# Optimization experiments

Hardware: AMD Instinct MI355X
Metric: run time of the kernel (lower is better)

The kernel has to match this reference:

```python
import jax, jax.numpy as jnp
import numpy as np

E, R, D, B = 1_000_000, 1_000, 64, 32_768
MARGIN = 1.0


def setup_inputs() -> dict:
    key = jax.random.key(0)
    ks = jax.random.split(key, 8)
    return {
        "ent_embeddings": jax.random.normal(ks[0], (E, D), dtype=jnp.float32) * (1.0 / np.sqrt(D)),
        "rel_matrices": jax.random.normal(ks[1], (R, D * D), dtype=jnp.float32) * (1.0 / D),
        "ph": jax.random.randint(ks[2], (B,), 0, E, dtype=jnp.int32),
        "pt": jax.random.randint(ks[3], (B,), 0, E, dtype=jnp.int32),
        "pr": jax.random.randint(ks[4], (B,), 0, R, dtype=jnp.int32),
        "nh": jax.random.randint(ks[5], (B,), 0, E, dtype=jnp.int32),
        "nt": jax.random.randint(ks[6], (B,), 0, E, dtype=jnp.int32),
        "nr": jax.random.randint(ks[7], (B,), 0, R, dtype=jnp.int32),
    }


def _score(ent, rel, h_idx, t_idx, r_idx):
    # gather: h,t -> [B,D]; r -> [B,D,D]
    h = ent[h_idx]
    t = ent[t_idx]
    r = rel[r_idx].reshape(-1, D, D)
    rt = jnp.einsum('bij,bj->bi', r, t)      # matmul(pr, pt): [B,D]
    # mean over D (keep_dims=False) then sum keepdims -> [B,1]
    return jnp.mean(h * rt, axis=1, keepdims=True)


def reference(ent_embeddings, rel_matrices, ph, pt, pr, nh, nt, nr):
    sp = _score(ent_embeddings, rel_matrices, ph, pt, pr)  # [B,1]
    sn = _score(ent_embeddings, rel_matrices, nh, nt, nr)  # [B,1]
    return jnp.sum(jnp.maximum(0.0, sn - sp + MARGIN))
```

## Files before the change

### kernel.cpp

```cpp
#include <hip/hip_runtime.h>


#define DIM 64
#define BATCH 32768
#define NREL 1000
#define NTASK (2 * BATCH)
#define BINCAP 128
#define RS 68
#define TS 36


__global__ __launch_bounds__(256) void scatter_kernel(
    const int* __restrict__ pr, const int* __restrict__ nr,
    int* __restrict__ cursors, int* __restrict__ bins,
    float* __restrict__ out)
{
    int t = blockIdx.x * 256 + threadIdx.x;
    int b = t & (BATCH - 1);
    int r = (t >> 15) ? nr[b] : pr[b];
    int c = atomicAdd(&cursors[r], 1);
    if (c < BINCAP) bins[r * BINCAP + c] = t;
    if (blockIdx.x == 0 && threadIdx.x == 0) *out = 0.f;
}

__global__ __launch_bounds__(256) void score_kernel(
    const float* __restrict__ ent, const float* __restrict__ rel,
    const int* __restrict__ ph, const int* __restrict__ pt,
    const int* __restrict__ nh, const int* __restrict__ nt,
    const int* __restrict__ cursors, const int* __restrict__ bins,
    float* __restrict__ scores)
{
    const int r = blockIdx.x;
    const int w = threadIdx.x >> 6;
    const int lane = threadIdx.x & 63;

    __shared__ float RT[DIM * RS];
    __shared__ float TT[4 * DIM * TS];

    const float4* rg = (const float4*)(rel + (size_t)r * (DIM * DIM));
    #pragma unroll
    for (int it = 0; it < 4; ++it) {
        int f = threadIdx.x + 256 * it;
        int i = f >> 4, jc = f & 15;
        float4 v = rg[f];
        RT[(4 * jc + 0) * RS + i] = v.x;
        RT[(4 * jc + 1) * RS + i] = v.y;
        RT[(4 * jc + 2) * RS + i] = v.z;
        RT[(4 * jc + 3) * RS + i] = v.w;
    }

    const int start = r * BINCAP;
    const int cnt = min(cursors[r], BINCAP);
    const int tb = start + w * 32;
    const int nv = min(32, cnt - w * 32);

    float* tt = &TT[w * (DIM * TS)];
    if (nv > 0) {
        int m = lane & 31;
        int ch = lane >> 5;
        int t = bins[tb + min(m, nv - 1)];
        int b = t & (BATCH - 1);
        int ti = (t >> 15) ? nt[b] : pt[b];
        const float4* tr = (const float4*)(ent + (size_t)ti * DIM);
        #pragma unroll
        for (int c = 0; c < 8; ++c) {
            float4 v = tr[ch * 8 + c];
            int j = ch * 32 + c * 4;
            tt[(j + 0) * TS + m] = v.x;
            tt[(j + 1) * TS + m] = v.y;
            tt[(j + 2) * TS + m] = v.z;
            tt[(j + 3) * TS + m] = v.w;
        }
    }
    __syncthreads();
    if (nv <= 0) return;

    const int mg = lane >> 3;
    const int ig = lane & 7;

    float acc[4][8];
    #pragma unroll
    for (int a = 0; a < 4; ++a)
        #pragma unroll
        for (int b = 0; b < 8; ++b) acc[a][b] = 0.f;

    const float* ttA = tt + mg * 4;
    const float* rtB = RT + ig * 8;
    #pragma unroll 2
    for (int j = 0; j < 64; ++j) {
        float4 Av = *(const float4*)(ttA + j * TS);
        float4 B0 = *(const float4*)(rtB + j * RS);
        float4 B1 = *(const float4*)(rtB + j * RS + 4);
        float A_[4] = {Av.x, Av.y, Av.z, Av.w};
        float B_[8] = {B0.x, B0.y, B0.z, B0.w, B1.x, B1.y, B1.z, B1.w};
        #pragma unroll
        for (int a = 0; a < 4; ++a)
            #pragma unroll
            for (int b = 0; b < 8; ++b)
                acc[a][b] = fmaf(A_[a], B_[b], acc[a][b]);
    }

    float sc[4]; int tk[4];
    #pragma unroll
    for (int a = 0; a < 4; ++a) {
        int m = mg * 4 + a;
        int t = bins[tb + min(m, nv - 1)];
        tk[a] = t;
        int b = t & (BATCH - 1);
        int hi = (t >> 15) ? nh[b] : ph[b];
        const float4* hr = (const float4*)(ent + (size_t)hi * DIM);
        float4 h0 = hr[ig * 2];
        float4 h1 = hr[ig * 2 + 1];
        float p = h0.x * acc[a][0] + h0.y * acc[a][1] +
                  h0.z * acc[a][2] + h0.w * acc[a][3] +
                  h1.x * acc[a][4] + h1.y * acc[a][5] +
                  h1.z * acc[a][6] + h1.w * acc[a][7];
        p += __shfl_xor(p, 1, 64);
        p += __shfl_xor(p, 2, 64);
        p += __shfl_xor(p, 4, 64);
        sc[a] = p;
    }
    if (ig == 0) {
        #pragma unroll
        for (int a = 0; a < 4; ++a)
            if (mg * 4 + a < nv) scores[tk[a]] = sc[a] * (1.0f / DIM);
    }
}

__global__ __launch_bounds__(256) void hinge_kernel(
    const float* __restrict__ scores, float* __restrict__ out)
{
    int b = blockIdx.x * 256 + threadIdx.x;
    float sp = scores[b];
    float sn = scores[BATCH + b];
    float v = fmaxf(0.f, sn - sp + 1.0f);
    #pragma unroll
    for (int off = 32; off > 0; off >>= 1)
        v += __shfl_xor(v, off, 64);
    __shared__ float red[4];
    int warp = threadIdx.x >> 6;
    int lane = threadIdx.x & 63;
    if (lane == 0) red[warp] = v;
    __syncthreads();
    if (threadIdx.x == 0)
        atomicAdd(out, red[0] + red[1] + red[2] + red[3]);
}

extern "C" void kernel_launch(void* const* d_in, const int* in_sizes, int n_in,
                              void* d_out, int out_size, void* d_ws, size_t ws_size,
                              hipStream_t stream) {
    const float* ent = (const float*)d_in[0];
    const float* rel = (const float*)d_in[1];
    const int* ph = (const int*)d_in[2];
    const int* pt = (const int*)d_in[3];
    const int* pr = (const int*)d_in[4];
    const int* nh = (const int*)d_in[5];
    const int* nt = (const int*)d_in[6];
    const int* nr = (const int*)d_in[7];
    float* out = (float*)d_out;

    char* ws = (char*)d_ws;
    int* cursors  = (int*)(ws + 0);
    int* bins     = (int*)(ws + 4096);
    float* scores = (float*)(ws + 516096);

    hipMemsetAsync(cursors, 0, 4096, stream);
    scatter_kernel<<<NTASK / 256, 256, 0, stream>>>(pr, nr, cursors, bins, out);
    score_kernel<<<NREL, 256, 0, stream>>>(ent, rel, ph, pt, nh, nt,
                                           cursors, bins, scores);
    hinge_kernel<<<BATCH / 256, 256, 0, stream>>>(scores, out);
}
```

Before: 341.9 us.

## Fuse hinge reduction into score kernel and pack gather indices into bins

The scatter kernel now stores the task id, tail index and head index together in an int4 bin entry. This removes the dependent index loads from the score kernel, which also issues its head-row loads before the matmul loop. The separate hinge kernel and scores buffer are gone: each triple's score is paired with its positive or negative partner through an atomicExch on a sentinel-initialised slot, and the hinge value is reduced per block into out. This saves a kernel launch and the scores round trip, at the cost of larger bin entries and extra global atomics.

```diff
diff --git a/kernel.cpp b/kernel.cpp
--- a/kernel.cpp
+++ b/kernel.cpp
@@ -8,27 +8,32 @@
 #define BINCAP 128
 #define RS 68
 #define TS 36
+#define SENT 0x7F800001u
 
 
 __global__ __launch_bounds__(256) void scatter_kernel(
-    const int* __restrict__ pr, const int* __restrict__ nr,
-    int* __restrict__ cursors, int* __restrict__ bins,
-    float* __restrict__ out)
+    const int* __restrict__ ph, const int* __restrict__ pt,
+    const int* __restrict__ pr, const int* __restrict__ nh,
+    const int* __restrict__ nt, const int* __restrict__ nr,
+    int* __restrict__ cursors, int4* __restrict__ bins,
+    unsigned int* __restrict__ pairs, float* __restrict__ out)
 {
     int t = blockIdx.x * 256 + threadIdx.x;
     int b = t & (BATCH - 1);
-    int r = (t >> 15) ? nr[b] : pr[b];
+    int side = t >> 15;
+    int r  = side ? nr[b] : pr[b];
+    int ti = side ? nt[b] : pt[b];
+    int hi = side ? nh[b] : ph[b];
     int c = atomicAdd(&cursors[r], 1);
-    if (c < BINCAP) bins[r * BINCAP + c] = t;
-    if (blockIdx.x == 0 && threadIdx.x == 0) *out = 0.f;
+    if (c < BINCAP) bins[r * BINCAP + c] = make_int4(t, ti, hi, 0);
+    pairs[b] = SENT;
+    if (t == 0) *out = 0.f;
 }
 
 __global__ __launch_bounds__(256) void score_kernel(
     const float* __restrict__ ent, const float* __restrict__ rel,
-    const int* __restrict__ ph, const int* __restrict__ pt,
-    const int* __restrict__ nh, const int* __restrict__ nt,
-    const int* __restrict__ cursors, const int* __restrict__ bins,
-    float* __restrict__ scores)
+    const int* __restrict__ cursors, const int4* __restrict__ bins,
+    unsigned int* __restrict__ pairs, float* __restrict__ out)
 {
     const int r = blockIdx.x;
     const int w = threadIdx.x >> 6;
@@ -36,6 +41,8 @@
 
     __shared__ float RT[DIM * RS];
     __shared__ float TT[4 * DIM * TS];
+    float* bsum = &RT[64];
+    if (threadIdx.x == 0) *bsum = 0.f;
 
     const float4* rg = (const float4*)(rel + (size_t)r * (DIM * DIM));
     #pragma unroll
@@ -58,10 +65,8 @@
     if (nv > 0) {
         int m = lane & 31;
         int ch = lane >> 5;
-        int t = bins[tb + min(m, nv - 1)];
-        int b = t & (BATCH - 1);
-        int ti = (t >> 15) ? nt[b] : pt[b];
-        const float4* tr = (const float4*)(ent + (size_t)ti * DIM);
+        int4 e = bins[tb + min(m, nv - 1)];
+        const float4* tr = (const float4*)(ent + (size_t)e.y * DIM);
         #pragma unroll
         for (int c = 0; c < 8; ++c) {
             float4 v = tr[ch * 8 + c];
@@ -73,77 +78,74 @@
         }
     }
     __syncthreads();
-    if (nv <= 0) return;
 
-    const int mg = lane >> 3;
-    const int ig = lane & 7;
+    if (nv > 0) {
+        const int mg = lane >> 3;
+        const int ig = lane & 7;
 
-    float acc[4][8];
-    #pragma unroll
-    for (int a = 0; a < 4; ++a)
+        float4 h0v[4], h1v[4]; int tk[4];
         #pragma unroll
-        for (int b = 0; b < 8; ++b) acc[a][b] = 0.f;
+        for (int a = 0; a < 4; ++a) {
+            int4 e = bins[tb + min(mg * 4 + a, nv - 1)];
+            tk[a] = e.x;
+            const float4* hr = (const float4*)(ent + (size_t)e.z * DIM);
+            h0v[a] = hr[ig * 2];
+            h1v[a] = hr[ig * 2 + 1];
+        }
 
-    const float* ttA = tt + mg * 4;
-    const float* rtB = RT + ig * 8;
-    #pragma unroll 2
-    for (int j = 0; j < 64; ++j) {
-        float4 Av = *(const float4*)(ttA + j * TS);
-        float4 B0 = *(const float4*)(rtB + j * RS);
-        float4 B1 = *(const float4*)(rtB + j * RS + 4);
-        float A_[4] = {Av.x, Av.y, Av.z, Av.w};
-        float B_[8] = {B0.x, B0.y, B0.z, B0.w, B1.x, B1.y, B1.z, B1.w};
+        float acc[4][8];
         #pragma unroll
         for (int a = 0; a < 4; ++a)
             #pragma unroll
-            for (int b = 0; b < 8; ++b)
-                acc[a][b] = fmaf(A_[a], B_[b], acc[a][b]);
+            for (int b = 0; b < 8; ++b) acc[a][b] = 0.f;
+
+        const float* ttA = tt + mg * 4;
+        const float* rtB = RT + ig * 8;
+        #pragma unroll 2
+        for (int j = 0; j < 64; ++j) {
+            float4 Av = *(const float4*)(ttA + j * TS);
+            float4 B0 = *(const float4*)(rtB + j * RS);
+            float4 B1 = *(const float4*)(rtB + j * RS + 4);
+            float A_[4] = {Av.x, Av.y, Av.z, Av.w};
+            float B_[8] = {B0.x, B0.y, B0.z, B0.w, B1.x, B1.y, B1.z, B1.w};
+            #pragma unroll
+            for (int a = 0; a < 4; ++a)
+                #pragma unroll
+                for (int b = 0; b < 8; ++b)
+                    acc[a][b] = fmaf(A_[a], B_[b], acc[a][b]);
+        }
+
+        float wsum = 0.f;
+        #pragma unroll
+        for (int a = 0; a < 4; ++a) {
+            float p = h0v[a].x * acc[a][0] + h0v[a].y * acc[a][1] +
+                      h0v[a].z * acc[a][2] + h0v[a].w * acc[a][3] +
+                      h1v[a].x * acc[a][4] + h1v[a].y * acc[a][5] +
+                      h1v[a].z * acc[a][6] + h1v[a].w * acc[a][7];
+            p += __shfl_xor(p, 1, 64);
+            p += __shfl_xor(p, 2, 64);
+            p += __shfl_xor(p, 4, 64);
+            if (ig == 0 && mg * 4 + a < nv) {
+                float s = p * (1.0f / DIM);
+                int b = tk[a] & (BATCH - 1);
+                int side = tk[a] >> 15;
+                unsigned int old = atomicExch(&pairs[b], __float_as_uint(s));
+                if (old != SENT) {
+                    float o = __uint_as_float(old);
+                    float sn = side ? s : o;
+                    float sp = side ? o : s;
+                    wsum += fmaxf(0.f, sn - sp + 1.0f);
+                }
+            }
+        }
+        #pragma unroll
+        for (int off = 1; off < 64; off <<= 1)
+            wsum += __shfl_xor(wsum, off, 64);
+        if (lane == 0 && wsum != 0.f) atomicAdd(bsum, wsum);
     }
 
-    float sc[4]; int tk[4];
-    #pragma unroll
-    for (int a = 0; a < 4; ++a) {
-        int m = mg * 4 + a;
-        int t = bins[tb + min(m, nv - 1)];
-        tk[a] = t;
-        int b = t & (BATCH - 1);
-        int hi = (t >> 15) ? nh[b] : ph[b];
-        const float4* hr = (const float4*)(ent + (size_t)hi * DIM);
-        float4 h0 = hr[ig * 2];
-        float4 h1 = hr[ig * 2 + 1];
-        float p = h0.x * acc[a][0] + h0.y * acc[a][1] +
-                  h0.z * acc[a][2] + h0.w * acc[a][3] +
-                  h1.x * acc[a][4] + h1.y * acc[a][5] +
-                  h1.z * acc[a][6] + h1.w * acc[a][7];
-        p += __shfl_xor(p, 1, 64);
-        p += __shfl_xor(p, 2, 64);
-        p += __shfl_xor(p, 4, 64);
-        sc[a] = p;
-    }
-    if (ig == 0) {
-        #pragma unroll
-        for (int a = 0; a < 4; ++a)
-            if (mg * 4 + a < nv) scores[tk[a]] = sc[a] * (1.0f / DIM);
-    }
-}
-
-__global__ __launch_bounds__(256) void hinge_kernel(
-    const float* __restrict__ scores, float* __restrict__ out)
-{
-    int b = blockIdx.x * 256 + threadIdx.x;
-    float sp = scores[b];
-    float sn = scores[BATCH + b];
-    float v = fmaxf(0.f, sn - sp + 1.0f);
-    #pragma unroll
-    for (int off = 32; off > 0; off >>= 1)
-        v += __shfl_xor(v, off, 64);
-    __shared__ float red[4];
-    int warp = threadIdx.x >> 6;
-    int lane = threadIdx.x & 63;
-    if (lane == 0) red[warp] = v;
     __syncthreads();
-    if (threadIdx.x == 0)
-        atomicAdd(out, red[0] + red[1] + red[2] + red[3]);
+    if (threadIdx.x == 0 && *bsum != 0.f) atomicAdd(out, *bsum);
 }
 
 extern "C" void kernel_launch(void* const* d_in, const int* in_sizes, int n_in,
@@ -160,13 +162,12 @@
     float* out = (float*)d_out;
 
     char* ws = (char*)d_ws;
-    int* cursors  = (int*)(ws + 0);
-    int* bins     = (int*)(ws + 4096);
-    float* scores = (float*)(ws + 516096);
+    int* cursors         = (int*)(ws + 0);
+    int4* bins           = (int4*)(ws + 4096);
+    unsigned int* pairs  = (unsigned int*)(ws + 2052096);
 
     hipMemsetAsync(cursors, 0, 4096, stream);
-    scatter_kernel<<<NTASK / 256, 256, 0, stream>>>(pr, nr, cursors, bins, out);
-    score_kernel<<<NREL, 256, 0, stream>>>(ent, rel, ph, pt, nh, nt,
-                                           cursors, bins, scores);
-    hinge_kernel<<<BATCH / 256, 256, 0, stream>>>(scores, out);
+    scatter_kernel<<<NTASK / 256, 256, 0, stream>>>(ph, pt, pr, nh, nt, nr,
+                                                    cursors, bins, pairs, out);
+    score_kernel<<<NREL, 256, 0, stream>>>(ent, rel, cursors, bins, pairs, out);
 }
```

Result: no change. 340.3 us (-0.5%).
